# Kernel tuning notes

Measured on AMD Instinct MI355X. Metric: run time of the kernel, lower is better.

## Reference

```python
import jax, jax.numpy as jnp
import numpy as np

N_NODES = 100000
N_EDGES = 400000
B = 1024
D_XD = 78
SEQ = 1000
EMB = 128
HID = 300
NF = 32
OUT_DIM = 128


def setup_inputs():
    key = jax.random.key(0)
    ks = jax.random.split(key, 40)
    rn = lambda k, s, sc=0.05: jax.random.normal(k, s, dtype=jnp.float32) * sc
    inp = {}
    inp['x'] = rn(ks[0], (N_NODES, D_XD), 1.0)
    inp['edge_index'] = jax.random.randint(ks[1], (2, N_EDGES), 0, N_NODES, dtype=jnp.int32)
    inp['batch'] = jnp.sort(jax.random.randint(ks[2], (N_NODES,), 0, B, dtype=jnp.int32))
    inp['target'] = jax.random.randint(ks[3], (B, SEQ), 0, 26, dtype=jnp.int32)
    inp['embs'] = rn(ks[4], (B * 13, 133), 1.0)
    inp['W1'] = rn(ks[5], (D_XD, D_XD)); inp['b1'] = jnp.zeros((D_XD,), jnp.float32)
    inp['W2'] = rn(ks[6], (D_XD, D_XD * 2)); inp['b2'] = jnp.zeros((D_XD * 2,), jnp.float32)
    inp['W3'] = rn(ks[7], (D_XD * 2, D_XD * 4)); inp['b3'] = jnp.zeros((D_XD * 4,), jnp.float32)
    inp['fc_g1_w'] = rn(ks[8], (D_XD * 4, 1024)); inp['fc_g1_b'] = jnp.zeros((1024,), jnp.float32)
    inp['fc_g2_w'] = rn(ks[9], (1024, OUT_DIM)); inp['fc_g2_b'] = jnp.zeros((OUT_DIM,), jnp.float32)
    inp['emb_xt'] = rn(ks[10], (26, EMB), 1.0)
    inp['conv_w'] = rn(ks[11], (NF, SEQ, 8)); inp['conv_b'] = jnp.zeros((NF,), jnp.float32)
    inp['fc1xt_w'] = rn(ks[12], (NF * 121, OUT_DIM)); inp['fc1xt_b'] = jnp.zeros((OUT_DIM,), jnp.float32)
    inp['fg_lin_w'] = rn(ks[13], (133, HID)); inp['fg_lin_b'] = jnp.zeros((HID,), jnp.float32)
    inp['Wq'] = rn(ks[14], (HID, HID)); inp['Wk'] = rn(ks[15], (HID, HID)); inp['Wv'] = rn(ks[16], (HID, HID))
    inp['ln_g'] = jnp.ones((HID,), jnp.float32); inp['ln_b'] = jnp.zeros((HID,), jnp.float32)
    inp['fg_out_w'] = rn(ks[17], (HID, OUT_DIM)); inp['fg_out_b'] = jnp.zeros((OUT_DIM,), jnp.float32)
    inp['fc1_w'] = rn(ks[18], (3 * OUT_DIM, 1024)); inp['fc1_b'] = jnp.zeros((1024,), jnp.float32)
    inp['fc2_w'] = rn(ks[19], (1024, 512)); inp['fc2_b'] = jnp.zeros((512,), jnp.float32)
    inp['out_w'] = rn(ks[20], (512, 1)); inp['out_b'] = jnp.zeros((1,), jnp.float32)
    return inp


def _gcn_conv(h_in, W, b, src, dst, dis):
    # PyG GCNConv: x' = D^-1/2 (A+I) D^-1/2 (X W) + b
    h = h_in @ W
    norm = dis[src] * dis[dst]  # [E]
    agg = jax.ops.segment_sum(h[src] * norm[:, None], dst, num_segments=h.shape[0])
    agg = agg + h * (dis * dis)[:, None]  # self-loop term
    return agg + b


def _forward(x, embs, W1, b1, W2, b2, W3, b3, fc_g1_w, fc_g1_b, fc_g2_w, fc_g2_b,
             emb_xt, conv_w, conv_b, fc1xt_w, fc1xt_b, fg_lin_w, fg_lin_b,
             Wq, Wk, Wv, ln_g, ln_b, fg_out_w, fg_out_b,
             fc1_w, fc1_b, fc2_w, fc2_b, out_w, out_b,
             edge_index, batch, target):
    src, dst = edge_index[0], edge_index[1]
    deg = jax.ops.segment_sum(jnp.ones_like(dst, jnp.float32), dst, num_segments=x.shape[0]) + 1.0
    dis = jax.lax.rsqrt(deg)
    h = jax.nn.relu(_gcn_conv(x, W1, b1, src, dst, dis))
    h = jax.nn.relu(_gcn_conv(h, W2, b2, src, dst, dis))
    h = jax.nn.relu(_gcn_conv(h, W3, b3, src, dst, dis))
    g = jax.ops.segment_max(h, batch, num_segments=B)  # global max pool
    g = jnp.where(jnp.isfinite(g), g, 0.0)
    g = jax.nn.relu(g @ fc_g1_w + fc_g1_b)
    g = g @ fc_g2_w + fc_g2_b  # dropout is identity at eval
    # protein branch: embedding + Conv1d(in=1000, out=32, k=8) over embed axis
    e = emb_xt[target]  # [B, SEQ, EMB]
    c = jax.lax.conv_general_dilated(e, conv_w, (1,), 'VALID',
                                     dimension_numbers=('NCH', 'OIH', 'NCH'))
    c = c + conv_b[None, :, None]  # [B, 32, 121]
    xt = c.reshape(B, NF * 121) @ fc1xt_w + fc1xt_b
    # functional-group prompt branch (KANO-style): linear -> self-attn -> LN -> gather row i*13
    f = (embs @ fg_lin_w + fg_lin_b).reshape(B, 13, HID)
    q = f @ Wq; k = f @ Wk; v = f @ Wv
    attn = jax.nn.softmax(jnp.einsum('bqd,bkd->bqk', q, k) / jnp.sqrt(jnp.float32(HID)), axis=-1)
    f2 = f + jnp.einsum('bqk,bkd->bqd', attn, v)
    mu = f2.mean(-1, keepdims=True)
    var = f2.var(-1, keepdims=True)
    f2 = (f2 - mu) * jax.lax.rsqrt(var + 1e-5) * ln_g + ln_b
    fg = f2[:, 0, :] @ fg_out_w + fg_out_b  # row i*13 per molecule
    xc = jnp.concatenate([g, xt, fg], axis=1)  # [B, 3*OUT_DIM]
    xc = jax.nn.relu(xc @ fc1_w + fc1_b)
    xc = jax.nn.relu(xc @ fc2_w + fc2_b)
    return xc @ out_w + out_b


def reference(x, edge_index, batch, target, embs, W1, b1, W2, b2, W3, b3,
              fc_g1_w, fc_g1_b, fc_g2_w, fc_g2_b, emb_xt, conv_w, conv_b,
              fc1xt_w, fc1xt_b, fg_lin_w, fg_lin_b, Wq, Wk, Wv, ln_g, ln_b,
              fg_out_w, fg_out_b, fc1_w, fc1_b, fc2_w, fc2_b, out_w, out_b):
    return _forward(x, embs, W1, b1, W2, b2, W3, b3, fc_g1_w, fc_g1_b, fc_g2_w, fc_g2_b,
                    emb_xt, conv_w, conv_b, fc1xt_w, fc1xt_b, fg_lin_w, fg_lin_b,
                    Wq, Wk, Wv, ln_g, ln_b, fg_out_w, fg_out_b,
                    fc1_w, fc1_b, fc2_w, fc2_b, out_w, out_b,
                    edge_index, batch, target)
```

## Files before the change

kernel.cpp:

```cpp
#include <hip/hip_runtime.h>
#include <hip/hip_bf16.h>
#include <math.h>

#define NNODES 100000
#define NEDGES 400000
#define NB     1024
#define SEQ    1000
#define HID    300
#define NBLK1  ((NNODES + 255) / 256)

typedef __attribute__((ext_vector_type(8))) short short8;
typedef __attribute__((ext_vector_type(4))) float f32x4;

__device__ __forceinline__ float bf_lo(unsigned int v) { return __uint_as_float(v << 16); }
__device__ __forceinline__ float bf_hi(unsigned int v) { return __uint_as_float(v & 0xffff0000u); }
__device__ __forceinline__ unsigned int bf_pack(float lo, float hi) {
    __hip_bfloat16 a = __float2bfloat16(lo), b = __float2bfloat16(hi);
    unsigned short ua = *(unsigned short*)&a, ub = *(unsigned short*)&b;
    return (unsigned int)ua | ((unsigned int)ub << 16);
}

__global__ void cvt_pad_kernel(const float* __restrict__ in, __hip_bfloat16* __restrict__ out,
                               int M, int K, int Kpad)
{
    long idx = (long)blockIdx.x * 256 + threadIdx.x;
    if (idx >= (long)M * Kpad) return;
    int m = idx / Kpad, k = idx % Kpad;
    out[idx] = __float2bfloat16(k < K ? in[(long)m * K + k] : 0.f);
}

__global__ void transpose_cvt_kernel(const float* __restrict__ in, __hip_bfloat16* __restrict__ out,
                                     int K, int N, int Kpad)
{
    long idx = (long)blockIdx.x * 256 + threadIdx.x;
    if (idx >= (long)N * Kpad) return;
    int n = idx / Kpad, k = idx % Kpad;
    out[idx] = __float2bfloat16(k < K ? in[(long)k * N + n] : 0.f);
}

struct TBatch {
    const float* src[12];
    __hip_bfloat16* dst[12];
    int K[12]; int N[12]; int Kpad[12];
    int bstart[13];
};

__global__ __launch_bounds__(256) void transpose_batch_kernel(TBatch tb)
{
    int blk = blockIdx.x;
    int d = 0;
    while (d < 11 && blk >= tb.bstart[d + 1]) ++d;
    long idx = (long)(blk - tb.bstart[d]) * 256 + threadIdx.x;
    long tot = (long)tb.N[d] * tb.Kpad[d];
    if (idx >= tot) return;
    int Kpad = tb.Kpad[d];
    int n = idx / Kpad, k = idx % Kpad;
    tb.dst[d][idx] = __float2bfloat16(k < tb.K[d] ? tb.src[d][(long)k * tb.N[d] + n] : 0.f);
}

__global__ __launch_bounds__(256) void gemm_bf16_kernel(
    const __hip_bfloat16* __restrict__ A, const __hip_bfloat16* __restrict__ Bt,
    const float* __restrict__ bias, void* __restrict__ C,
    int M, int N, int Kpad, int lda, int ldc, int Npad_out,
    int relu, int outbf, int chunk)
{
    __shared__ __align__(16) __hip_bfloat16 As[64][40];
    __shared__ __align__(16) __hip_bfloat16 Bs[64][40];
    int tid = threadIdx.x;
    int wave = tid >> 6, lane = tid & 63;
    int wm = wave >> 1, wn = wave & 1;
    int quad = lane >> 4, l16 = lane & 15;
    int row0 = blockIdx.y * 64, col0 = blockIdx.x * 64;

    int kbeg = 0, kend = Kpad;
    if (chunk > 0) { kbeg = blockIdx.z * chunk; kend = kbeg + chunk; if (kend > Kpad) kend = Kpad; }

    f32x4 acc[2][2];
    #pragma unroll
    for (int i = 0; i < 2; ++i)
        #pragma unroll
        for (int j = 0; j < 2; ++j) acc[i][j] = (f32x4){0.f, 0.f, 0.f, 0.f};

    int r = tid >> 2, cch = (tid & 3) * 8;

    for (int k0 = kbeg; k0 < kend; k0 += 32) {
        uint4 av = {0u, 0u, 0u, 0u};
        if (row0 + r < M) av = *(const uint4*)(A + (size_t)(row0 + r) * lda + k0 + cch);
        *(uint4*)(&As[r][cch]) = av;
        uint4 bv = {0u, 0u, 0u, 0u};
        if (col0 + r < N) bv = *(const uint4*)(Bt + (size_t)(col0 + r) * Kpad + k0 + cch);
        *(uint4*)(&Bs[r][cch]) = bv;
        __syncthreads();

        short8 a0 = *(const short8*)(&As[wm * 32 + l16][quad * 8]);
        short8 a1 = *(const short8*)(&As[wm * 32 + 16 + l16][quad * 8]);
        short8 b0 = *(const short8*)(&Bs[wn * 32 + l16][quad * 8]);
        short8 b1 = *(const short8*)(&Bs[wn * 32 + 16 + l16][quad * 8]);
        acc[0][0] = __builtin_amdgcn_mfma_f32_16x16x32_bf16(a0, b0, acc[0][0], 0, 0, 0);
        acc[0][1] = __builtin_amdgcn_mfma_f32_16x16x32_bf16(a0, b1, acc[0][1], 0, 0, 0);
        acc[1][0] = __builtin_amdgcn_mfma_f32_16x16x32_bf16(a1, b0, acc[1][0], 0, 0, 0);
        acc[1][1] = __builtin_amdgcn_mfma_f32_16x16x32_bf16(a1, b1, acc[1][1], 0, 0, 0);
        __syncthreads();
    }

    #pragma unroll
    for (int ti = 0; ti < 2; ++ti) {
        int rbase = row0 + wm * 32 + ti * 16 + quad * 4;
        #pragma unroll
        for (int tj = 0; tj < 2; ++tj) {
            int cc = col0 + wn * 32 + tj * 16 + l16;
            if (cc >= Npad_out) continue;
            #pragma unroll
            for (int reg = 0; reg < 4; ++reg) {
                int rr = rbase + reg;
                if (rr >= M) continue;
                float v = acc[ti][tj][reg];
                if (chunk > 0) {
                    if (cc < N) atomicAdd((float*)C + (size_t)rr * ldc + cc, v);
                } else {
                    float ov = 0.f;
                    if (cc < N) {
                        if (bias) v += bias[cc];
                        if (relu) v = fmaxf(v, 0.f);
                        ov = v;
                    }
                    if (outbf) ((__hip_bfloat16*)C)[(size_t)rr * ldc + cc] = __float2bfloat16(ov);
                    else       ((float*)C)[(size_t)rr * ldc + cc] = ov;
                }
            }
        }
    }
}

static void launch_gemm_bf16(const __hip_bfloat16* A, const __hip_bfloat16* Bt, const float* bias,
                             void* C, int M, int N, int Kpad, int lda, int ldc, int Npad_out,
                             int relu, int outbf, int splitz, hipStream_t stream)
{
    int cover = N > Npad_out ? N : Npad_out;
    int chunk = (splitz > 1) ? (Kpad / splitz) : 0;
    dim3 grid((cover + 63) / 64, (M + 63) / 64, splitz > 1 ? splitz : 1);
    gemm_bf16_kernel<<<grid, 256, 0, stream>>>(A, Bt, bias, C, M, N, Kpad, lda, ldc, Npad_out,
                                               relu, outbf, chunk);
}

__global__ void deg_kernel(const int* __restrict__ dst, int* __restrict__ deg, int E)
{
    int e = blockIdx.x * 256 + threadIdx.x;
    if (e < E) atomicAdd(&deg[dst[e]], 1);
}

__global__ void dis_kernel(const int* __restrict__ deg, float* __restrict__ dis,
                           float* __restrict__ selfc, int n)
{
    int i = blockIdx.x * 256 + threadIdx.x;
    if (i < n) {
        float d = (float)deg[i] + 1.0f;
        float r = 1.0f / sqrtf(d);
        dis[i] = r;
        selfc[i] = r * r;
    }
}

__global__ __launch_bounds__(256) void scan_p1(const int* __restrict__ deg,
                                               int* __restrict__ off, int* __restrict__ bsum)
{
    __shared__ int s[256];
    int tid = threadIdx.x;
    int i = blockIdx.x * 256 + tid;
    int v = (i < NNODES) ? deg[i] : 0;
    s[tid] = v;
    __syncthreads();
    #pragma unroll
    for (int d = 1; d < 256; d <<= 1) {
        int t = (tid >= d) ? s[tid - d] : 0;
        __syncthreads();
        s[tid] += t;
        __syncthreads();
    }
    if (i < NNODES) off[i] = s[tid] - v;
    if (tid == 255) bsum[blockIdx.x] = s[255];
}

__global__ __launch_bounds__(512) void scan_p2(int* __restrict__ bsum)
{
    __shared__ int s[512];
    int tid = threadIdx.x;
    int v = (tid < NBLK1) ? bsum[tid] : 0;
    s[tid] = v;
    __syncthreads();
    #pragma unroll
    for (int d = 1; d < 512; d <<= 1) {
        int t = (tid >= d) ? s[tid - d] : 0;
        __syncthreads();
        s[tid] += t;
        __syncthreads();
    }
    if (tid < NBLK1) bsum[tid] = s[tid] - v;
}

__global__ __launch_bounds__(256) void scan_p3(int* __restrict__ off, const int* __restrict__ bsum,
                                               int* __restrict__ cur)
{
    int i = blockIdx.x * 256 + threadIdx.x;
    if (i < NNODES) {
        int v = off[i] + bsum[blockIdx.x];
        off[i] = v;
        cur[i] = v;
    }
    if (i == NNODES) off[NNODES] = NEDGES;
}

__global__ void fill_csr_kernel(const int* __restrict__ src, const int* __restrict__ dst,
                                const float* __restrict__ dis, int* __restrict__ cur,
                                int* __restrict__ csr_src, float* __restrict__ csr_w, int E)
{
    int e = blockIdx.x * 256 + threadIdx.x;
    if (e >= E) return;
    int s = src[e], d = dst[e];
    int p = atomicAdd(&cur[d], 1);
    csr_src[p] = s;
    csr_w[p] = dis[s] * dis[d];
}

__global__ __launch_bounds__(256) void gcn_agg2(
    const __hip_bfloat16* __restrict__ Tin, const int* __restrict__ off,
    const int* __restrict__ csr_src, const float* __restrict__ csr_w,
    const float* __restrict__ selfc, __hip_bfloat16* __restrict__ out,
    int half, int nc)
{
    int wave = threadIdx.x >> 6, lane = threadIdx.x & 63;
    int node = blockIdx.x * 4 + wave;
    if (node >= NNODES) return;
    const unsigned int* Tp = (const unsigned int*)Tin;
    unsigned int* Op = (unsigned int*)out;
    size_t rb = (size_t)node * half;
    bool m0 = lane < half;
    bool m1 = (nc > 1) && (lane + 64 < half);
    float sc = selfc[node];
    float a0x = 0.f, a0y = 0.f, a1x = 0.f, a1y = 0.f;
    float b0x = 0.f, b0y = 0.f, b1x = 0.f, b1y = 0.f;
    if (m0) { unsigned int v = Tp[rb + lane];      a0x = bf_lo(v) * sc; a0y = bf_hi(v) * sc; }
    if (m1) { unsigned int v = Tp[rb + lane + 64]; a1x = bf_lo(v) * sc; a1y = bf_hi(v) * sc; }
    int s0 = off[node], s1 = off[node + 1];
    int e = s0;
    for (; e + 2 <= s1; e += 2) {
        int i0 = csr_src[e], i1 = csr_src[e + 1];
        float w0 = csr_w[e], w1 = csr_w[e + 1];
        size_t p0 = (size_t)i0 * half, p1 = (size_t)i1 * half;
        unsigned int v00 = 0u, v01 = 0u, v10 = 0u, v11 = 0u;
        if (m0) { v00 = Tp[p0 + lane]; v10 = Tp[p1 + lane]; }
        if (m1) { v01 = Tp[p0 + lane + 64]; v11 = Tp[p1 + lane + 64]; }
        if (m0) {
            a0x += bf_lo(v00) * w0; a0y += bf_hi(v00) * w0;
            b0x += bf_lo(v10) * w1; b0y += bf_hi(v10) * w1;
        }
        if (m1) {
            a1x += bf_lo(v01) * w0; a1y += bf_hi(v01) * w0;
            b1x += bf_lo(v11) * w1; b1y += bf_hi(v11) * w1;
        }
    }
    if (e < s1) {
        int i0 = csr_src[e];
        float w0 = csr_w[e];
        size_t p0 = (size_t)i0 * half;
        if (m0) { unsigned int v = Tp[p0 + lane];      a0x += bf_lo(v) * w0; a0y += bf_hi(v) * w0; }
        if (m1) { unsigned int v = Tp[p0 + lane + 64]; a1x += bf_lo(v) * w0; a1y += bf_hi(v) * w0; }
    }
    if (m0) Op[rb + lane]      = bf_pack(a0x + b0x, a0y + b0y);
    if (m1) Op[rb + lane + 64] = bf_pack(a1x + b1x, a1y + b1y);
}

__global__ __launch_bounds__(256) void pool_max_bf16(
    const __hip_bfloat16* __restrict__ H, const int* __restrict__ batch,
    __hip_bfloat16* __restrict__ g)
{
    int b = blockIdx.x;
    int lo = 0, hi = NNODES;
    while (lo < hi) { int mid = (lo + hi) >> 1; if (batch[mid] < b) lo = mid + 1; else hi = mid; }
    int s = lo;
    hi = NNODES;
    while (lo < hi) { int mid = (lo + hi) >> 1; if (batch[mid] < b + 1) lo = mid + 1; else hi = mid; }
    int e = lo;
    int tid = threadIdx.x;
    if (tid < 160) {
        const unsigned int* Hp = (const unsigned int*)H;
        float mx = 0.f, my = 0.f;
        for (int i = s; i < e; ++i) {
            unsigned int v = Hp[(size_t)i * 160 + tid];
            mx = fmaxf(mx, bf_lo(v));
            my = fmaxf(my, bf_hi(v));
        }
        ((unsigned int*)g)[(size_t)b * 160 + tid] = bf_pack(mx, my);
    }
}

__global__ void conv_transpose_kernel(const float* __restrict__ w, __hip_bfloat16* __restrict__ wt)
{
    int idx = blockIdx.x * 256 + threadIdx.x;
    if (idx >= 256000) return;
    int o = idx / 8000;
    int rem = idx - o * 8000;
    int i = rem >> 3, k = rem & 7;
    wt[i * 256 + o * 8 + k] = __float2bfloat16(w[idx]);
}

__global__ __launch_bounds__(256) void conv_agg_kernel(
    const __hip_bfloat16* __restrict__ cwt, const int* __restrict__ target,
    __hip_bfloat16* __restrict__ aggw)
{
    __shared__ int tb_s[SEQ];
    __shared__ int cnt[26];
    __shared__ int boff[27];
    __shared__ int curs[26];
    __shared__ int bucket[SEQ];
    int b = blockIdx.x, tid = threadIdx.x;
    const int* tb = target + b * SEQ;
    if (tid < 26) cnt[tid] = 0;
    __syncthreads();
    for (int i = tid; i < SEQ; i += 256) {
        int a = tb[i];
        tb_s[i] = a;
        atomicAdd(&cnt[a], 1);
    }
    __syncthreads();
    if (tid == 0) {
        int run = 0;
        for (int a = 0; a < 26; ++a) { boff[a] = run; curs[a] = run; run += cnt[a]; }
        boff[26] = run;
    }
    __syncthreads();
    for (int i = tid; i < SEQ; i += 256) {
        int a = tb_s[i];
        int p = atomicAdd(&curs[a], 1);
        bucket[p] = i;
    }
    __syncthreads();
    for (int a = 0; a < 26; ++a) {
        int s = boff[a], e = boff[a + 1];
        float acc0 = 0.f, acc1 = 0.f, acc2 = 0.f, acc3 = 0.f;
        int j = s;
        for (; j + 4 <= e; j += 4) {
            acc0 += __bfloat162float(cwt[bucket[j]     * 256 + tid]);
            acc1 += __bfloat162float(cwt[bucket[j + 1] * 256 + tid]);
            acc2 += __bfloat162float(cwt[bucket[j + 2] * 256 + tid]);
            acc3 += __bfloat162float(cwt[bucket[j + 3] * 256 + tid]);
        }
        for (; j < e; ++j)
            acc0 += __bfloat162float(cwt[bucket[j] * 256 + tid]);
        aggw[(size_t)b * 6656 + a * 256 + tid] = __float2bfloat16((acc0 + acc1) + (acc2 + acc3));
    }
}

__global__ __launch_bounds__(128) void conv_wc_kernel(
    const float* __restrict__ emb, const float* __restrict__ w_fc, float* __restrict__ Wc)
{
    int o = blockIdx.x;
    int ak = blockIdx.y;
    int a = ak >> 3, k = ak & 7;
    int j = threadIdx.x;
    const float* wp = w_fc + (long)(o * 121) * 128 + j;
    const float* ep = emb + a * 128 + k;
    float s = 0.f;
    #pragma unroll 11
    for (int t = 0; t < 121; ++t) s += ep[t] * wp[t * 128];
    Wc[(long)(a * 256 + o * 8 + k) * 128 + j] = s;
}

__global__ void xtb_init_kernel(const float* __restrict__ b_fc, float* __restrict__ xtb)
{
    xtb[threadIdx.x] = b_fc[threadIdx.x];
}

__global__ __launch_bounds__(128) void convb_fold_kernel(
    const float* __restrict__ w_fc, const float* __restrict__ conv_b, float* __restrict__ xtb)
{
    int o = blockIdx.x, j = threadIdx.x;
    const float* wp = w_fc + (long)(o * 121) * 128 + j;
    float s = 0.f;
    for (int t = 0; t < 121; ++t) s += wp[t * 128];
    atomicAdd(&xtb[j], s * conv_b[o]);
}

__global__ void xc_convbias_kernel(const float* __restrict__ xtb, float* __restrict__ xc)
{
    int idx = blockIdx.x * 256 + threadIdx.x;
    if (idx >= NB * 128) return;
    int b = idx >> 7, j = idx & 127;
    xc[(long)b * 384 + 128 + j] = xtb[j];
}

__global__ __launch_bounds__(256) void attn_ln_kernel(
    const __hip_bfloat16* __restrict__ Fb, const __hip_bfloat16* __restrict__ Kf,
    const __hip_bfloat16* __restrict__ Vf, const __hip_bfloat16* __restrict__ q0,
    const float* __restrict__ ln_g, const float* __restrict__ ln_b,
    __hip_bfloat16* __restrict__ out)
{
    int b = blockIdx.x, tid = threadIdx.x;
    __shared__ float qs[HID];
    __shared__ float sc[13];
    __shared__ float red[256];
    __shared__ float red2[256];
    __shared__ float rowv[HID];
    __shared__ float mean_s, inv_s;

    for (int d = tid; d < HID; d += 256) qs[d] = __bfloat162float(q0[(size_t)b * 320 + d]);
    __syncthreads();
    if (tid < 208) {
        int k = tid >> 4, sub = tid & 15;
        const __hip_bfloat16* kr = Kf + ((size_t)b * 13 + k) * 320;
        float p = 0.f;
        for (int d = sub; d < HID; d += 16) p += qs[d] * __bfloat162float(kr[d]);
        red[tid] = p;
    }
    __syncthreads();
    if (tid < 208 && (tid & 15) == 0) {
        float s = 0.f;
        #pragma unroll
        for (int j = 0; j < 16; ++j) s += red[tid + j];
        sc[tid >> 4] = s * 0.0577350269189626f;
    }
    __syncthreads();
    if (tid == 0) {
        float mx = sc[0];
        for (int k = 1; k < 13; ++k) mx = fmaxf(mx, sc[k]);
        float ssum = 0.f;
        for (int k = 0; k < 13; ++k) { float e = expf(sc[k] - mx); sc[k] = e; ssum += e; }
        float inv = 1.0f / ssum;
        for (int k = 0; k < 13; ++k) sc[k] *= inv;
    }
    __syncthreads();
    for (int d = tid; d < HID; d += 256) {
        float v = __bfloat162float(Fb[((size_t)b * 13) * 320 + d]);
        #pragma unroll
        for (int k = 0; k < 13; ++k)
            v += sc[k] * __bfloat162float(Vf[((size_t)b * 13 + k) * 320 + d]);
        rowv[d] = v;
    }
    __syncthreads();
    float s1 = 0.f, s2 = 0.f;
    for (int d = tid; d < HID; d += 256) { float v = rowv[d]; s1 += v; s2 += v * v; }
    red[tid] = s1; red2[tid] = s2;
    __syncthreads();
    for (int s = 128; s > 0; s >>= 1) {
        if (tid < s) { red[tid] += red[tid + s]; red2[tid] += red2[tid + s]; }
        __syncthreads();
    }
    if (tid == 0) {
        float mean = red[0] / (float)HID;
        float var = red2[0] / (float)HID - mean * mean;
        mean_s = mean;
        inv_s = 1.0f / sqrtf(var + 1e-5f);
    }
    __syncthreads();
    for (int d = tid; d < 320; d += 256) {
        float v = 0.f;
        if (d < HID) v = (rowv[d] - mean_s) * inv_s * ln_g[d] + ln_b[d];
        out[(size_t)b * 320 + d] = __float2bfloat16(v);
    }
}

__global__ __launch_bounds__(256) void final_out_kernel(
    const float* __restrict__ X, const float* __restrict__ w,
    const float* __restrict__ bias, float* __restrict__ out)
{
    int b = blockIdx.x, tid = threadIdx.x;
    __shared__ float red[256];
    float p = X[(long)b * 512 + tid] * w[tid] + X[(long)b * 512 + tid + 256] * w[tid + 256];
    red[tid] = p;
    __syncthreads();
    for (int s = 128; s > 0; s >>= 1) {
        if (tid < s) red[tid] += red[tid + s];
        __syncthreads();
    }
    if (tid == 0) out[b] = red[0] + bias[0];
}

extern "C" void kernel_launch(void* const* d_in, const int* in_sizes, int n_in,
                              void* d_out, int out_size, void* d_ws, size_t ws_size,
                              hipStream_t stream)
{
    const float* x        = (const float*)d_in[0];
    const int*   ei       = (const int*)d_in[1];
    const int*   batch    = (const int*)d_in[2];
    const int*   target   = (const int*)d_in[3];
    const float* embs     = (const float*)d_in[4];
    const float* W1       = (const float*)d_in[5];
    const float* b1       = (const float*)d_in[6];
    const float* W2       = (const float*)d_in[7];
    const float* b2       = (const float*)d_in[8];
    const float* W3       = (const float*)d_in[9];
    const float* b3       = (const float*)d_in[10];
    const float* fc_g1_w  = (const float*)d_in[11];
    const float* fc_g1_b  = (const float*)d_in[12];
    const float* fc_g2_w  = (const float*)d_in[13];
    const float* fc_g2_b  = (const float*)d_in[14];
    const float* emb_xt   = (const float*)d_in[15];
    const float* conv_w   = (const float*)d_in[16];
    const float* conv_b   = (const float*)d_in[17];
    const float* fc1xt_w  = (const float*)d_in[18];
    const float* fc1xt_b  = (const float*)d_in[19];
    const float* fg_lin_w = (const float*)d_in[20];
    const float* fg_lin_b = (const float*)d_in[21];
    const float* Wq       = (const float*)d_in[22];
    const float* Wk       = (const float*)d_in[23];
    const float* Wv       = (const float*)d_in[24];
    const float* ln_g     = (const float*)d_in[25];
    const float* ln_b     = (const float*)d_in[26];
    const float* fg_out_w = (const float*)d_in[27];
    const float* fg_out_b = (const float*)d_in[28];
    const float* fc1_w    = (const float*)d_in[29];
    const float* fc1_b    = (const float*)d_in[30];
    const float* fc2_w    = (const float*)d_in[31];
    const float* fc2_b    = (const float*)d_in[32];
    const float* out_w    = (const float*)d_in[33];
    const float* out_b    = (const float*)d_in[34];

    const int* src = ei;
    const int* dst = ei + NEDGES;
    typedef __hip_bfloat16 bf;

    char* p = (char*)d_ws;
    auto alloc = [&](size_t bytes) { char* r = p; p += (bytes + 255) & ~(size_t)255; return r; };
    bf*   xb      = (bf*)alloc((size_t)NNODES * 96 * 2);
    bf*   T       = (bf*)alloc((size_t)NNODES * 160 * 2);
    bf*   H       = (bf*)alloc((size_t)NNODES * 320 * 2);
    int*  deg     = (int*)alloc(NNODES * 4);
    float* dis    = (float*)alloc(NNODES * 4);
    float* selfc  = (float*)alloc(NNODES * 4);
    int*  off     = (int*)alloc((NNODES + 1) * 4);
    int*  bsum    = (int*)alloc(512 * 4);
    int*  csr_src = (int*)alloc(NEDGES * 4);
    float* csr_w  = (float*)alloc(NEDGES * 4);
    bf*   w1t     = (bf*)alloc(78 * 96 * 2);
    bf*   w2t     = (bf*)alloc(156 * 96 * 2);
    bf*   w3t     = (bf*)alloc(312 * 160 * 2);
    bf*   fcg1t   = (bf*)alloc(1024 * 320 * 2);
    bf*   fcg2t   = (bf*)alloc(128 * 1024 * 2);
    bf*   fglint  = (bf*)alloc(300 * 160 * 2);
    bf*   wkt     = (bf*)alloc(300 * 320 * 2);
    bf*   wvt     = (bf*)alloc(300 * 320 * 2);
    bf*   wqt     = (bf*)alloc(300 * 320 * 2);
    bf*   fgoutt  = (bf*)alloc(128 * 320 * 2);
    bf*   fc1t    = (bf*)alloc(1024 * 384 * 2);
    bf*   fc2t    = (bf*)alloc(512 * 1024 * 2);
    bf*   g       = (bf*)alloc((size_t)NB * 320 * 2);
    bf*   G1b     = (bf*)alloc((size_t)NB * 1024 * 2);
    bf*   embsb   = (bf*)alloc((size_t)NB * 13 * 160 * 2);
    bf*   Fbuf    = (bf*)alloc((size_t)NB * 13 * 320 * 2);
    bf*   Kbuf    = (bf*)alloc((size_t)NB * 13 * 320 * 2);
    bf*   Vbuf    = (bf*)alloc((size_t)NB * 13 * 320 * 2);
    bf*   Qbuf    = (bf*)alloc((size_t)NB * 320 * 2);
    bf*   f2row   = (bf*)alloc((size_t)NB * 320 * 2);
    float* xc     = (float*)alloc((size_t)NB * 384 * 4);
    bf*   xcb     = (bf*)alloc((size_t)NB * 384 * 2);
    float* F2     = (float*)alloc((size_t)NB * 512 * 4);
    bf*   cwt     = (bf*)alloc(256000 * 2);
    bf*   aggwb   = (bf*)alloc((size_t)NB * 6656 * 2);
    float* Wc     = (float*)alloc((size_t)6656 * 128 * 4);
    bf*   Wct     = (bf*)alloc((size_t)128 * 6656 * 2);
    float* xtb    = (float*)alloc(128 * 4);

    hipMemsetAsync(deg, 0, NNODES * sizeof(int), stream);
    deg_kernel<<<(NEDGES + 255) / 256, 256, 0, stream>>>(dst, deg, NEDGES);
    dis_kernel<<<(NNODES + 255) / 256, 256, 0, stream>>>(deg, dis, selfc, NNODES);
    scan_p1<<<NBLK1, 256, 0, stream>>>(deg, off, bsum);
    scan_p2<<<1, 512, 0, stream>>>(bsum);
    scan_p3<<<NBLK1, 256, 0, stream>>>(off, bsum, deg);
    fill_csr_kernel<<<(NEDGES + 255) / 256, 256, 0, stream>>>(src, dst, dis, deg, csr_src, csr_w, NEDGES);

    {
        TBatch tb;
        const float* srcs[12] = {W1, W2, W3, fc_g1_w, fc_g2_w, fg_lin_w, Wk, Wv, Wq, fg_out_w, fc1_w, fc2_w};
        bf* dsts[12]          = {w1t, w2t, w3t, fcg1t, fcg2t, fglint, wkt, wvt, wqt, fgoutt, fc1t, fc2t};
        int Ks[12]    = {78, 78, 156, 312, 1024, 133, 300, 300, 300, 300, 384, 1024};
        int Ns[12]    = {78, 156, 312, 1024, 128, 300, 300, 300, 300, 128, 1024, 512};
        int Kpads[12] = {96, 96, 160, 320, 1024, 160, 320, 320, 320, 320, 384, 1024};
        int bs = 0;
        for (int i = 0; i < 12; ++i) {
            tb.src[i] = srcs[i]; tb.dst[i] = dsts[i];
            tb.K[i] = Ks[i]; tb.N[i] = Ns[i]; tb.Kpad[i] = Kpads[i];
            tb.bstart[i] = bs;
            bs += (int)(((long)Ns[i] * Kpads[i] + 255) / 256);
        }
        tb.bstart[12] = bs;
        transpose_batch_kernel<<<bs, 256, 0, stream>>>(tb);
    }
    cvt_pad_kernel<<<((long)NNODES * 96 + 255) / 256, 256, 0, stream>>>(x, xb, NNODES, 78, 96);
    cvt_pad_kernel<<<((long)NB * 13 * 160 + 255) / 256, 256, 0, stream>>>(embs, embsb, NB * 13, 133, 160);

    int agrid = (NNODES + 3) / 4;
    gcn_agg2<<<agrid, 256, 0, stream>>>(xb, off, csr_src, csr_w, selfc, T, 48, 1);
    launch_gemm_bf16(T, w1t, b1, H, NNODES, 78, 96, 96, 96, 96, 1, 1, 1, stream);

    gcn_agg2<<<agrid, 256, 0, stream>>>(H, off, csr_src, csr_w, selfc, T, 48, 1);
    launch_gemm_bf16(T, w2t, b2, H, NNODES, 156, 96, 96, 160, 160, 1, 1, 1, stream);

    gcn_agg2<<<agrid, 256, 0, stream>>>(H, off, csr_src, csr_w, selfc, T, 80, 2);
    launch_gemm_bf16(T, w3t, b3, H, NNODES, 312, 160, 160, 320, 320, 1, 1, 1, stream);

    pool_max_bf16<<<NB, 256, 0, stream>>>(H, batch, g);
    launch_gemm_bf16(g, fcg1t, fc_g1_b, G1b, NB, 1024, 320, 320, 1024, 1024, 1, 1, 1, stream);
    launch_gemm_bf16(G1b, fcg2t, fc_g2_b, xc, NB, 128, 1024, 1024, 384, 128, 0, 0, 1, stream);

    conv_transpose_kernel<<<(256000 + 255) / 256, 256, 0, stream>>>(conv_w, cwt);
    conv_agg_kernel<<<NB, 256, 0, stream>>>(cwt, target, aggwb);
    conv_wc_kernel<<<dim3(32, 208), 128, 0, stream>>>(emb_xt, fc1xt_w, Wc);
    transpose_cvt_kernel<<<((long)128 * 6656 + 255) / 256, 256, 0, stream>>>(Wc, Wct, 6656, 128, 6656);
    xtb_init_kernel<<<1, 128, 0, stream>>>(fc1xt_b, xtb);
    convb_fold_kernel<<<32, 128, 0, stream>>>(fc1xt_w, conv_b, xtb);
    xc_convbias_kernel<<<(NB * 128 + 255) / 256, 256, 0, stream>>>(xtb, xc);
    launch_gemm_bf16(aggwb, Wct, nullptr, xc + 128, NB, 128, 6656, 6656, 384, 128, 0, 0, 8, stream);

    launch_gemm_bf16(embsb, fglint, fg_lin_b, Fbuf, NB * 13, 300, 160, 160, 320, 320, 0, 1, 1, stream);
    launch_gemm_bf16(Fbuf, wkt, nullptr, Kbuf, NB * 13, 300, 320, 320, 320, 320, 0, 1, 1, stream);
    launch_gemm_bf16(Fbuf, wvt, nullptr, Vbuf, NB * 13, 300, 320, 320, 320, 320, 0, 1, 1, stream);
    launch_gemm_bf16(Fbuf, wqt, nullptr, Qbuf, NB, 300, 320, 13 * 320, 320, 320, 0, 1, 1, stream);
    attn_ln_kernel<<<NB, 256, 0, stream>>>(Fbuf, Kbuf, Vbuf, Qbuf, ln_g, ln_b, f2row);
    launch_gemm_bf16(f2row, fgoutt, fg_out_b, xc + 256, NB, 128, 320, 320, 384, 128, 0, 0, 1, stream);

    cvt_pad_kernel<<<((long)NB * 384 + 255) / 256, 256, 0, stream>>>(xc, xcb, NB, 384, 384);
    launch_gemm_bf16(xcb, fc1t, fc1_b, G1b, NB, 1024, 384, 384, 1024, 1024, 1, 1, 1, stream);
    launch_gemm_bf16(G1b, fc2t, fc2_b, F2, NB, 512, 1024, 1024, 512, 512, 1, 0, 1, stream);
    final_out_kernel<<<NB, 256, 0, stream>>>(F2, out_w, out_b, (float*)d_out);
}
```

Baseline: 777.3 us.

## Add 128x64-tile MFMA GEMM for GCN layers and wave-split conv aggregation

Adds a dedicated bf16 MFMA GEMM with 128-row tiles and a fixed bias+ReLU bf16 epilogue, used for the three large GCN feature transforms over 100k nodes, so each block reuses its loaded B tile across more rows. It also rewrites the conv aggregation so each wave gathers a different subset of sequence positions using 8-byte vector loads of four bf16 values, then combines partial sums through shared memory. The aggregation change adds two block barriers per amino-acid bucket. The new GEMM has no software pipelining and no split-K, and it uses a non-ASCII identifier ('bféin') that some compilers may reject.

```diff
diff --git a/kernel.cpp b/kernel.cpp
--- a/kernel.cpp
+++ b/kernel.cpp
@@ -141,6 +141,81 @@
     dim3 grid((cover + 63) / 64, (M + 63) / 64, splitz > 1 ? splitz : 1);
     gemm_bf16_kernel<<<grid, 256, 0, stream>>>(A, Bt, bias, C, M, N, Kpad, lda, ldc, Npad_out,
                                                relu, outbf, chunk);
+}
+
+__global__ __launch_bounds__(256) void gemm_big_kernel(
+    const __hip_bfloat16* __restrict__ A, const __hip_bfloat16* __restrict__ Bt,
+    const float* __restrict__ bias, __hip_bfloat16* __restrict__ C,
+    int M, int N, int Kpad, int lda, int ldc, int Npad_out)
+{
+    __shared__ __align__(16) __hip_bfloat16 As[128][40];
+    __shared__ __align__(16) __hip_bfloat16 Bs[64][40];
+    int tid = threadIdx.x;
+    int wave = tid >> 6, lane = tid & 63;
+    int wm = wave >> 1, wn = wave & 1;
+    int quad = lane >> 4, l16 = lane & 15;
+    int row0 = blockIdx.y * 128, col0 = blockIdx.x * 64;
+
+    f32x4 acc[4][2];
+    #pragma unroll
+    for (int i = 0; i < 4; ++i)
+        #pragma unroll
+        for (int j = 0; j < 2; ++j) acc[i][j] = (f32x4){0.f, 0.f, 0.f, 0.f};
+
+    int r = tid >> 2, cch = (tid & 3) * 8;
+
+    for (int k0 = 0; k0 < Kpad; k0 += 32) {
+        uint4 av0 = {0u, 0u, 0u, 0u}, av1 = {0u, 0u, 0u, 0u}, bv = {0u, 0u, 0u, 0u};
+        if (row0 + r < M)      av0 = *(const uint4*)(A + (size_t)(row0 + r) * lda + k0 + cch);
+        if (row0 + r + 64 < M) av1 = *(const uint4*)(A + (size_t)(row0 + r + 64) * lda + k0 + cch);
+        if (col0 + r < N)      bv  = *(const uint4*)(Bt + (size_t)(col0 + r) * Kpad + k0 + cch);
+        *(uint4*)(&As[r][cch]) = av0;
+        *(uint4*)(&As[r + 64][cch]) = av1;
+        *(uint4*)(&Bs[r][cch]) = bv;
+        __syncthreads();
+
+        short8 af[4], bféin[2];
+        #pragma unroll
+        for (int i = 0; i < 4; ++i)
+            af[i] = *(const short8*)(&As[wm * 64 + i * 16 + l16][quad * 8]);
+        #pragma unroll
+        for (int j = 0; j < 2; ++j)
+            bféin[j] = *(const short8*)(&Bs[wn * 32 + j * 16 + l16][quad * 8]);
+        #pragma unroll
+        for (int i = 0; i < 4; ++i)
+            #pragma unroll
+            for (int j = 0; j < 2; ++j)
+                acc[i][j] = __builtin_amdgcn_mfma_f32_16x16x32_bf16(af[i], bféin[j], acc[i][j], 0, 0, 0);
+        __syncthreads();
+    }
+
+    #pragma unroll
+    for (int ti = 0; ti < 4; ++ti) {
+        int rbase = row0 + wm * 64 + ti * 16 + quad * 4;
+        #pragma unroll
+        for (int tj = 0; tj < 2; ++tj) {
+            int cc = col0 + wn * 32 + tj * 16 + l16;
+            if (cc >= Npad_out) continue;
+            #pragma unroll
+            for (int reg = 0; reg < 4; ++reg) {
+                int rr = rbase + reg;
+                if (rr >= M) continue;
+                float v = acc[ti][tj][reg];
+                float ov = 0.f;
+                if (cc < N) ov = fmaxf(v + bias[cc], 0.f);
+                C[(size_t)rr * ldc + cc] = __float2bfloat16(ov);
+            }
+        }
+    }
+}
+
+static void launch_gemm_big(const __hip_bfloat16* A, const __hip_bfloat16* Bt, const float* bias,
+                            __hip_bfloat16* C, int M, int N, int Kpad, int lda, int ldc,
+                            int Npad_out, hipStream_t stream)
+{
+    int cover = N > Npad_out ? N : Npad_out;
+    dim3 grid((cover + 63) / 64, (M + 127) / 128);
+    gemm_big_kernel<<<grid, 256, 0, stream>>>(A, Bt, bias, C, M, N, Kpad, lda, ldc, Npad_out);
 }
 
 __global__ void deg_kernel(const int* __restrict__ dst, int* __restrict__ deg, int E)
@@ -313,7 +388,9 @@
     __shared__ int boff[27];
     __shared__ int curs[26];
     __shared__ int bucket[SEQ];
+    __shared__ float comb[3][256];
     int b = blockIdx.x, tid = threadIdx.x;
+    int wave = tid >> 6, lane = tid & 63;
     const int* tb = target + b * SEQ;
     if (tid < 26) cnt[tid] = 0;
     __syncthreads();
@@ -335,19 +412,43 @@
         bucket[p] = i;
     }
     __syncthreads();
+
+    const uint2* cw = (const uint2*)cwt;
+    uint2* aw = (uint2*)aggw;
     for (int a = 0; a < 26; ++a) {
         int s = boff[a], e = boff[a + 1];
-        float acc0 = 0.f, acc1 = 0.f, acc2 = 0.f, acc3 = 0.f;
-        int j = s;
-        for (; j + 4 <= e; j += 4) {
-            acc0 += __bfloat162float(cwt[bucket[j]     * 256 + tid]);
-            acc1 += __bfloat162float(cwt[bucket[j + 1] * 256 + tid]);
-            acc2 += __bfloat162float(cwt[bucket[j + 2] * 256 + tid]);
-            acc3 += __bfloat162float(cwt[bucket[j + 3] * 256 + tid]);
-        }
-        for (; j < e; ++j)
-            acc0 += __bfloat162float(cwt[bucket[j] * 256 + tid]);
-        aggw[(size_t)b * 6656 + a * 256 + tid] = __float2bfloat16((acc0 + acc1) + (acc2 + acc3));
+        float x0 = 0.f, x1 = 0.f, x2 = 0.f, x3 = 0.f;
+        float y0 = 0.f, y1 = 0.f, y2 = 0.f, y3 = 0.f;
+        int j = s + wave;
+        for (; j + 4 < e; j += 8) {
+            uint2 v = cw[(size_t)bucket[j] * 64 + lane];
+            uint2 u = cw[(size_t)bucket[j + 4] * 64 + lane];
+            x0 += bf_lo(v.x); x1 += bf_hi(v.x); x2 += bf_lo(v.y); x3 += bf_hi(v.y);
+            y0 += bf_lo(u.x); y1 += bf_hi(u.x); y2 += bf_lo(u.y); y3 += bf_hi(u.y);
+        }
+        if (j < e) {
+            uint2 v = cw[(size_t)bucket[j] * 64 + lane];
+            x0 += bf_lo(v.x); x1 += bf_hi(v.x); x2 += bf_lo(v.y); x3 += bf_hi(v.y);
+        }
+        x0 += y0; x1 += y1; x2 += y2; x3 += y3;
+        if (wave > 0) {
+            comb[wave - 1][lane * 4 + 0] = x0;
+            comb[wave - 1][lane * 4 + 1] = x1;
+            comb[wave - 1][lane * 4 + 2] = x2;
+            comb[wave - 1][lane * 4 + 3] = x3;
+        }
+        __syncthreads();
+        if (wave == 0) {
+            x0 += comb[0][lane * 4 + 0] + comb[1][lane * 4 + 0] + comb[2][lane * 4 + 0];
+            x1 += comb[0][lane * 4 + 1] + comb[1][lane * 4 + 1] + comb[2][lane * 4 + 1];
+            x2 += comb[0][lane * 4 + 2] + comb[1][lane * 4 + 2] + comb[2][lane * 4 + 2];
+            x3 += comb[0][lane * 4 + 3] + comb[1][lane * 4 + 3] + comb[2][lane * 4 + 3];
+            uint2 o;
+            o.x = bf_pack(x0, x1);
+            o.y = bf_pack(x2, x3);
+            aw[(size_t)b * 1664 + a * 64 + lane] = o;
+        }
+        __syncthreads();
     }
 }
 
@@ -590,13 +691,13 @@
 
     int agrid = (NNODES + 3) / 4;
     gcn_agg2<<<agrid, 256, 0, stream>>>(xb, off, csr_src, csr_w, selfc, T, 48, 1);
-    launch_gemm_bf16(T, w1t, b1, H, NNODES, 78, 96, 96, 96, 96, 1, 1, 1, stream);
+    launch_gemm_big(T, w1t, b1, H, NNODES, 78, 96, 96, 96, 96, stream);
 
     gcn_agg2<<<agrid, 256, 0, stream>>>(H, off, csr_src, csr_w, selfc, T, 48, 1);
-    launch_gemm_bf16(T, w2t, b2, H, NNODES, 156, 96, 96, 160, 160, 1, 1, 1, stream);
+    launch_gemm_big(T, w2t, b2, H, NNODES, 156, 96, 96, 160, 160, stream);
 
     gcn_agg2<<<agrid, 256, 0, stream>>>(H, off, csr_src, csr_w, selfc, T, 80, 2);
-    launch_gemm_bf16(T, w3t, b3, H, NNODES, 312, 160, 160, 320, 320, 1, 1, 1, stream);
+    launch_gemm_big(T, w3t, b3, H, NNODES, 312, 160, 160, 320, 320, stream);
 
     pool_max_bf16<<<NB, 256, 0, stream>>>(H, batch, g);
     launch_gemm_bf16(g, fcg1t, fc_g1_b, G1b, NB, 1024, 320, 320, 1024, 1024, 1, 1, 1, stream);
```

Measured after the change: 760.0 us. -2.2%, faster.
